# Kernel tuning notes

Hardware: AMD Instinct MI355X
Metric: run time of the kernel (lower is better)

## Reference

```python
import jax, jax.numpy as jnp
import numpy as np
from math import factorial, sqrt

# ---------------- irreps utilities ----------------
def parse(s):
    out = []
    for tok in s.split('+'):
        tok = tok.strip()
        mul, ir = (tok.split('x') if 'x' in tok else ('1', tok))
        out.append((int(mul), int(ir[:-1]), 1 if ir[-1] == 'e' else -1))
    return out

def irdim(ir):
    return sum(m * (2 * l + 1) for m, l, p in ir)

def slices(ir):
    s, o = [], 0
    for m, l, p in ir:
        s.append((o, m, l, p)); o += m * (2 * l + 1)
    return s

# ---------------- real Clebsch-Gordan coefficients ----------------
def _cgc(j1, m1, j2, m2, j3, m3):
    if m1 + m2 != m3:
        return 0.0
    f = factorial
    pre = sqrt((2 * j3 + 1) * f(j3 + j1 - j2) * f(j3 - j1 + j2) * f(j1 + j2 - j3) / f(j1 + j2 + j3 + 1))
    pre *= sqrt(f(j3 + m3) * f(j3 - m3) * f(j1 - m1) * f(j1 + m1) * f(j2 - m2) * f(j2 + m2))
    s = 0.0
    for k in range(max(0, j2 - j3 - m1, j1 - j3 + m2), min(j1 + j2 - j3, j1 - m1, j2 + m2) + 1):
        s += (-1) ** k / (f(k) * f(j1 + j2 - j3 - k) * f(j1 - m1 - k) * f(j2 + m2 - k) * f(j3 - j2 + m1 + k) * f(j3 - j1 - m2 + k))
    return pre * s

def _c2r(l):
    # complex -> real spherical-harmonic change of basis
    q = np.zeros((2 * l + 1, 2 * l + 1), dtype=complex); r2 = 1 / np.sqrt(2)
    q[l, l] = 1.0
    for mu in range(1, l + 1):
        q[mu + l, mu + l] = (-1) ** mu * r2; q[mu + l, -mu + l] = r2
        q[-mu + l, -mu + l] = 1j * r2;       q[-mu + l, mu + l] = -1j * (-1) ** mu * r2
    return q

_CGMEM = {}
def cg_real(l1, l2, l3):
    key = (l1, l2, l3)
    if key in _CGMEM:
        return _CGMEM[key]
    C = np.zeros((2 * l1 + 1, 2 * l2 + 1, 2 * l3 + 1))
    for m1 in range(-l1, l1 + 1):
        for m2 in range(-l2, l2 + 1):
            if abs(m1 + m2) <= l3:
                C[m1 + l1, m2 + l2, m1 + m2 + l3] = _cgc(l1, m1, l2, m2, l3, m1 + m2)
    T = np.einsum('am,bn,co,mno->abc', _c2r(l1), _c2r(l2), np.conj(_c2r(l3)), C)
    R = T.real if np.abs(T.real).sum() >= np.abs(T.imag).sum() else T.imag
    _CGMEM[key] = np.ascontiguousarray(R)
    return _CGMEM[key]

# ---------------- equivariant ops ----------------
def tp_paths(ir1, ir2, iro):
    P = []
    for (o1, m1, l1, p1) in slices(ir1):
        for (o2, m2, l2, p2) in slices(ir2):
            for (oo, mo, lo, po) in slices(iro):
                if po == p1 * p2 and abs(l1 - l2) <= lo <= l1 + l2:
                    P.append((o1, m1, l1, o2, m2, l2, oo, mo, lo))
    return P

def tp_numel(P):
    return sum(m1 * m2 * mo for (_, m1, _, _, m2, _, _, mo, _) in P)

def tp_apply(ir1, ir2, iro, x1, x2, w):
    # FullyConnectedTensorProduct with per-row (shared_weights=False) weights w:[E, numel]
    P = tp_paths(ir1, ir2, iro)
    out = jnp.zeros((x1.shape[0], irdim(iro)), x1.dtype)
    fan = {}
    for p in P:
        fan[p[6]] = fan.get(p[6], 0) + p[1] * p[4]
    off = 0
    for (o1, m1, l1, o2, m2, l2, oo, mo, lo) in P:
        cg = jnp.asarray(cg_real(l1, l2, lo), x1.dtype)
        a = x1[:, o1:o1 + m1 * (2 * l1 + 1)].reshape(-1, m1, 2 * l1 + 1)
        b = x2[:, o2:o2 + m2 * (2 * l2 + 1)].reshape(-1, m2, 2 * l2 + 1)
        ww = w[:, off:off + m1 * m2 * mo].reshape(-1, m1, m2, mo); off += m1 * m2 * mo
        r = jnp.einsum('eui,evj,euvw,ijk->ewk', a, b, ww, cg) / np.sqrt(fan[oo])
        out = out.at[:, oo:oo + mo * (2 * lo + 1)].add(r.reshape(-1, mo * (2 * lo + 1)))
    return out

def lin_pairs(iri, iro):
    return [(si, so) for si in slices(iri) for so in slices(iro) if si[2] == so[2] and si[3] == so[3]]

def lin_numel(iri, iro):
    return sum(si[1] * so[1] for si, so in lin_pairs(iri, iro))

def lin_apply(iri, iro, x, w):
    # o3.Linear: per-irrep channel mixing with fan-in normalization
    out = jnp.zeros((x.shape[0], irdim(iro)), x.dtype)
    pairs = lin_pairs(iri, iro)
    fan = {}
    for si, so in pairs:
        fan[so[0]] = fan.get(so[0], 0) + si[1]
    off = 0
    for (oi, mi, li, pi), (oo, mo, lo, po) in pairs:
        W = w[off:off + mi * mo].reshape(mi, mo); off += mi * mo
        xb = x[:, oi:oi + mi * (2 * li + 1)].reshape(-1, mi, 2 * li + 1)
        r = jnp.einsum('eui,uv->evi', xb, W) / np.sqrt(fan[oo])
        out = out.at[:, oo:oo + mo * (2 * lo + 1)].add(r.reshape(-1, mo * (2 * lo + 1)))
    return out

def act_apply(ir, acts, x):
    # tanh on scalar irreps only (flags in acts), identity elsewhere
    parts = []
    for (o, m, l, p), a in zip(slices(ir), acts):
        b = x[:, o:o + m * (2 * l + 1)]
        parts.append(jnp.tanh(b) if a else b)
    return jnp.concatenate(parts, axis=1)

def fc_apply(x, w, dims):
    # e3nn FullyConnectedNet: relu MLP with 1/sqrt(fan_in) weight normalization
    off, h = 0, x
    for i in range(len(dims) - 1):
        di, do = dims[i], dims[i + 1]
        W = w[off:off + di * do].reshape(di, do); off += di * do
        h = (h @ W) / np.sqrt(di)
        if i < len(dims) - 2:
            h = jax.nn.relu(h)
    return h

# ---------------- module irreps (from V_theta.__init__) ----------------
IRR_IN = parse('2x0e')
IRR_SH = parse('1x0e+1x1o+1x2e')
MID1 = parse('8x0e+8x1o+8x2e')
MID2 = parse('8x0e+8x0o+8x1e+8x1o+8x2e+8x2o')
IRR_HH = parse('4x0e+2x1o+2x1o+1x0e+1x1e+1x2e')
IRR_CC = parse('9x0e+6x1o+3x2e+6x1o+' + '1x0e+1x1e+1x2e+' * 4 + '1x1o+1x2o+1x3o+' * 2 + '3x2e+' + '1x1o+1x2o+1x3o+' * 2 + '1x0e+1x1e+1x2e+1x3e+1x4e')
IRR_CH = parse('6x0e+3x1o+4x1o+' + '1x0e+1x1e+1x2e+' * 2 + '2x2e+1x1o+1x2o+1x3o')
SCR = parse('32x0e+1x2e'); SCR2 = parse('1x0e+1x2e'); G1 = parse('32x0e'); G2 = parse('3x0e')
ACT2 = [1, 0, 0]; ACT3 = [1, 1, 0, 0, 0, 0]
P1 = tp_paths(IRR_IN, IRR_SH, MID1); P2 = tp_paths(MID1, IRR_SH, MID2); PB = tp_paths(MID2, MID2, MID2)
EMB_N = 16
FC1D = [1, EMB_N, EMB_N, EMB_N, tp_numel(P1)]
FC2D = [1, EMB_N, EMB_N, EMB_N, tp_numel(P2)]
FCBD = [1, EMB_N, EMB_N, EMB_N, tp_numel(PB)]

def fcsz(d):
    return sum(d[i] * d[i + 1] for i in range(len(d) - 1))

N_NODES, N_EDGES, N_BOND, SCALING = 10000, 100000, 1000, 0.2


def setup_inputs() -> dict:
    key = jax.random.key(0)
    ks = jax.random.split(key, 32)
    nrm = lambda i, shp: jax.random.normal(ks[i], shp, jnp.float32)
    return {
        'f_in': nrm(0, (N_NODES, 2)),
        'sh': nrm(1, (N_EDGES, 9)),
        'emb': jax.random.uniform(ks[2], (N_EDGES, 1), jnp.float32),
        'num_neighbors': jnp.full((1,), 10.0, jnp.float32),
        'w_lin1': nrm(3, (lin_numel(IRR_IN, IRR_IN),)),
        'w_lin2': nrm(4, (lin_numel(MID1, MID1),)),
        'w_lin3': nrm(5, (lin_numel(MID2, MID2),)),
        'w_linCC': nrm(6, (lin_numel(MID2, IRR_CC),)),
        'w_linHH': nrm(7, (lin_numel(MID2, IRR_HH),)),
        'w_linCH': nrm(8, (lin_numel(MID2, IRR_CH),)),
        'w_linC': nrm(9, (lin_numel(MID2, IRR_CC),)),
        'w_linH': nrm(10, (lin_numel(MID2, IRR_HH),)),
        'w_screen1': nrm(11, (lin_numel(MID2, SCR),)),
        'w_screen2': nrm(12, (lin_numel(SCR, SCR2),)),
        'w_gap1': nrm(13, (lin_numel(MID2, G1),)),
        'w_gap2': nrm(14, (lin_numel(G1, G2),)),
        'w_fc1': nrm(15, (fcsz(FC1D),)),
        'w_fc2': nrm(16, (fcsz(FC2D),)),
        'w_fcb': nrm(17, (fcsz(FCBD),)),
        'edge_src': jax.random.randint(ks[18], (N_EDGES,), 0, N_NODES),
        'edge_dst': jax.random.randint(ks[19], (N_EDGES,), 0, N_NODES),
        'HH_ind': jax.random.randint(ks[20], (N_BOND,), 0, N_EDGES),
        'CC_ind': jax.random.randint(ks[21], (N_BOND,), 0, N_EDGES),
        'CH_ind': jax.random.randint(ks[22], (N_BOND,), 0, N_EDGES),
        'num_nodes': N_NODES,
    }


def reference(f_in, sh, emb, num_neighbors, w_lin1, w_lin2, w_lin3, w_linCC, w_linHH, w_linCH, w_linC, w_linH, w_screen1, w_screen2, w_gap1, w_gap2, w_fc1, w_fc2, w_fcb, edge_src, edge_dst, HH_ind, CC_ind, CH_ind, num_nodes):
    inv = 1.0 / jnp.sqrt(num_neighbors)  # .div(num_neighbors**0.5)
    # layer 1: linear + tanh, gather -> TP with per-edge weights -> scatter-add
    x = jnp.tanh(lin_apply(IRR_IN, IRR_IN, f_in, w_lin1))
    ef = tp_apply(IRR_IN, IRR_SH, MID1, x[edge_src], sh, fc_apply(emb, w_fc1, FC1D))
    x = jax.ops.segment_sum(ef, edge_dst, num_segments=num_nodes) * inv
    x = act_apply(MID1, ACT2, lin_apply(MID1, MID1, x, w_lin2))
    # layer 2
    ef = tp_apply(MID1, IRR_SH, MID2, x[edge_src], sh, fc_apply(emb, w_fc2, FC2D))
    x = jax.ops.segment_sum(ef, edge_dst, num_segments=num_nodes) * inv
    x = act_apply(MID2, ACT3, lin_apply(MID2, MID2, x, w_lin3))
    # bond-level tensor products on edge subsets
    def bond(ind):
        return tp_apply(MID2, MID2, MID2, x[edge_src[ind]], x[edge_dst[ind]], fc_apply(emb[ind], w_fcb, FCBD))
    HHf, CCf, CHf = bond(HH_ind), bond(CC_ind), bond(CH_ind)
    eHH = lin_apply(MID2, IRR_HH, act_apply(MID2, ACT3, HHf), w_linHH)
    eCC = lin_apply(MID2, IRR_CC, act_apply(MID2, ACT3, CCf), w_linCC)
    eCH = lin_apply(MID2, IRR_CH, act_apply(MID2, ACT3, CHf), w_linCH)
    nC = lin_apply(MID2, IRR_CC, x, w_linC)
    nH = lin_apply(MID2, IRR_HH, x, w_linH)
    screen = lin_apply(SCR, SCR2, act_apply(SCR, [1, 0], lin_apply(MID2, SCR, x, w_screen1)), w_screen2)
    def gap(F):
        return lin_apply(G1, G2, jnp.tanh(lin_apply(MID2, G1, F, w_gap1)), w_gap2)
    s = SCALING
    # order: H, C, HH, CH, CC, screen, gap[CC], gap[HH], gap[CH]
    return (nH * s, nC * s, eHH * s, eCH * s, eCC * s, screen, gap(CCf), gap(HHf), gap(CHf))
```

## Files before the change

kernel.cpp:

```cpp
#include <hip/hip_runtime.h>
#include <hip/hip_bf16.h>

typedef __hip_bfloat16 bf16_t;

#define N_NODES 10000
#define N_EDGES 100000
#define N_BONDS 1000
#define RPW 4

__device__ __forceinline__ float bf2f(bf16_t v){ return __bfloat162float(v); }
__device__ __forceinline__ bf16_t f2bf(float v){ return __float2bfloat16(v); }
__device__ __forceinline__ int iabs(int x){ return x<0?-x:x; }

constexpr bool cg_nz(int l1,int l2,int l3,int i,int j,int k){
  int m1=i-l1, m2=j-l2, m3=k-l3;
  int neg=(m1<0)+(m2<0)+(m3<0);
  if (((neg ^ (l1+l2+l3)) & 1)!=0) return false;
  int a1=m1<0?-m1:m1, a2=m2<0?-m2:m2, a3=m3<0?-m3:m3;
  return (a3==a1+a2)||(a3==a1-a2)||(a3==a2-a1);
}

__device__ __forceinline__ void stout(void* out, size_t idx, float v, bool f32o){
  if (f32o) ((float*)out)[idx]=v;
  else      ((bf16_t*)out)[idx]=f2bf(v);
}

__global__ void detect_k(const unsigned short* nnb_raw, int* flag){
  *flag = (nnb_raw[0]==0x4120) ? 0 : 1;
}

struct CvtArgs {
  const void* src[19];
  float* dst[19];
  int n[19];
};

__global__ __launch_bounds__(256) void convert_k(CvtArgs a, const int* flag){
  bool f32 = (*flag)!=0;
  int tid = blockIdx.x*256+threadIdx.x;
  int nth = gridDim.x*256;
  for(int t=0;t<19;++t){
    int n=a.n[t];
    float* d=a.dst[t];
    if (f32){
      const float* s=(const float*)a.src[t];
      for(int i=tid;i<n;i+=nth) d[i]=s[i];
    } else {
      const bf16_t* s=(const bf16_t*)a.src[t];
      for(int i=tid;i<n;i+=nth) d[i]=bf2f(s[i]);
    }
  }
}

__global__ __launch_bounds__(256) void csr_count_k(const int* __restrict__ edst, int* __restrict__ cnt){
  int e=blockIdx.x*256+threadIdx.x; if(e>=N_EDGES) return;
  atomicAdd(&cnt[edst[e]],1);
}

__global__ __launch_bounds__(256) void csr_scan_k(const int* __restrict__ cnt,
    int* __restrict__ rowptr, int* __restrict__ pos){
  __shared__ int ssum[256];
  int t=threadIdx.x;
  int base=t*40;
  int s=0;
  for(int i=0;i<40;++i){ int idx=base+i; s += (idx<N_NODES)? cnt[idx]:0; }
  ssum[t]=s; __syncthreads();
  if(t==0){ int run=0; for(int i=0;i<256;++i){ int v=ssum[i]; ssum[i]=run; run+=v; } }
  __syncthreads();
  int run=ssum[t];
  for(int i=0;i<40;++i){
    int idx=base+i;
    if(idx<N_NODES){ rowptr[idx]=run; pos[idx]=run; run+=cnt[idx]; }
  }
  if(t==255) rowptr[N_NODES]=run;
}

__global__ __launch_bounds__(256) void csr_scatter_k(const int* __restrict__ edst,
    int* __restrict__ pos, int* __restrict__ sorted){
  int e=blockIdx.x*256+threadIdx.x; if(e>=N_EDGES) return;
  int p=atomicAdd(&pos[edst[e]],1);
  sorted[p]=e;
}

__device__ __forceinline__ double dfact(int n){
  const double F[11]={1.,1.,2.,6.,24.,120.,720.,5040.,40320.,362880.,3628800.};
  return F[n];
}

__device__ double cgc_d(int j1,int m1,int j2,int m2,int j3,int m3){
  if (m1+m2!=m3) return 0.0;
  double pre = sqrt((double)(2*j3+1)*dfact(j3+j1-j2)*dfact(j3-j1+j2)*dfact(j1+j2-j3)/dfact(j1+j2+j3+1));
  pre *= sqrt(dfact(j3+m3)*dfact(j3-m3)*dfact(j1-m1)*dfact(j1+m1)*dfact(j2-m2)*dfact(j2+m2));
  int k0 = max(0, max(j2-j3-m1, j1-j3+m2));
  int k1 = min(j1+j2-j3, min(j1-m1, j2+m2));
  double s=0.0;
  for(int k=k0;k<=k1;++k)
    s += ((k&1)?-1.0:1.0)/(dfact(k)*dfact(j1+j2-j3-k)*dfact(j1-m1-k)*dfact(j2+m2-k)*dfact(j3-j2+m1+k)*dfact(j3-j1-m2+k));
  return pre*s;
}

__device__ void c2r_d(int l,int a,int m,double&re,double&im){
  re=0.0; im=0.0;
  const double r2 = 0.7071067811865475244;
  int mu = a-l;
  if (mu==0){ if (m==l) re=1.0; return; }
  if (mu>0){
    if (m==l+mu) re = (mu&1)? -r2 : r2;
    else if (m==l-mu) re = r2;
  } else {
    int nu=-mu;
    if (m==l-nu) im = r2;
    else if (m==l+nu) im = (nu&1)? r2 : -r2;
  }
}

__global__ __launch_bounds__(128) void cg_init_k(float* cg){
  int b=blockIdx.x;
  int l1=b/9, l2=(b/3)%3, l3=b%3;
  if (l3 < iabs(l1-l2) || l3 > l1+l2) return;
  int n1=2*l1+1,n2=2*l2+1,n3=2*l3+1,n=n1*n2*n3;
  __shared__ double sRe[125], sIm[125];
  __shared__ int sPick;
  int t=threadIdx.x;
  if (t<n){
    int a=t/(n2*n3), bb=(t/n3)%n2, c=t%n3;
    double re=0.0, im=0.0;
    for(int m1=0;m1<n1;++m1){
      double q1r,q1i; c2r_d(l1,a,m1,q1r,q1i);
      if (q1r==0.0 && q1i==0.0) continue;
      for(int m2=0;m2<n2;++m2){
        double q2r,q2i; c2r_d(l2,bb,m2,q2r,q2i);
        if (q2r==0.0 && q2i==0.0) continue;
        int m3=(m1-l1)+(m2-l2)+l3;
        if (m3<0||m3>=n3) continue;
        double q3r,q3i; c2r_d(l3,c,m3,q3r,q3i); q3i=-q3i;
        double C = cgc_d(l1,m1-l1,l2,m2-l2,l3,m3-l3);
        if (C==0.0) continue;
        double ar = q1r*q2r - q1i*q2i;
        double ai = q1r*q2i + q1i*q2r;
        re += (ar*q3r - ai*q3i)*C;
        im += (ar*q3i + ai*q3r)*C;
      }
    }
    sRe[t]=re; sIm[t]=im;
  }
  __syncthreads();
  if (t==0){
    double s1=0.0,s2=0.0;
    for(int i=0;i<n;++i){ s1+=fabs(sRe[i]); s2+=fabs(sIm[i]); }
    sPick = (s1>=s2)?1:0;
  }
  __syncthreads();
  if (t<n) cg[b*125+t] = (float)(sPick? sRe[t] : sIm[t]);
}

__global__ __launch_bounds__(256) void nodeA_k(const float* __restrict__ fin,
                                               const float* __restrict__ w,
                                               float* __restrict__ x1){
  int n=blockIdx.x*256+threadIdx.x; if(n>=N_NODES) return;
  float f0=fin[2*n], f1=fin[2*n+1];
  const float r2=0.70710678f;
  x1[2*n]   = tanhf((f0*w[0]+f1*w[2])*r2);
  x1[2*n+1] = tanhf((f0*w[1]+f1*w[3])*r2);
}

__device__ __forceinline__ void mlp16(float e, const float* w, float* h){
  float a[16];
  #pragma unroll
  for(int j=0;j<16;++j) a[j]=fmaxf(e*w[j],0.f);
  float b[16];
  #pragma unroll
  for(int j=0;j<16;++j){
    float s=0.f;
    #pragma unroll
    for(int i=0;i<16;++i) s+=a[i]*w[16+i*16+j];
    b[j]=fmaxf(s*0.25f,0.f);
  }
  #pragma unroll
  for(int j=0;j<16;++j){
    float s=0.f;
    #pragma unroll
    for(int i=0;i<16;++i) s+=b[i]*w[272+i*16+j];
    h[j]=fmaxf(s*0.25f,0.f);
  }
}

__global__ __launch_bounds__(256) void hmlp_k(const float* __restrict__ emb,
    const float* __restrict__ wfc, float* __restrict__ H, int E){
  __shared__ float sw[528];
  for(int t=threadIdx.x;t<528;t+=256) sw[t]=wfc[t];
  __syncthreads();
  int e=blockIdx.x*256+threadIdx.x; if(e>=E) return;
  float h[16]; mlp16(emb[e], sw, h);
  float4* H4=(float4*)(H+(size_t)e*16);
  #pragma unroll
  for(int q=0;q<4;++q) H4[q]=make_float4(h[4*q],h[4*q+1],h[4*q+2],h[4*q+3]);
}

__global__ __launch_bounds__(256) void hb_k(const float* __restrict__ emb,
    const float* __restrict__ wfc, const int* __restrict__ i0,
    const int* __restrict__ i1, const int* __restrict__ i2,
    float* __restrict__ HB){
  __shared__ float sw[528];
  for(int t=threadIdx.x;t<528;t+=256) sw[t]=wfc[t];
  __syncthreads();
  int t=blockIdx.x*256+threadIdx.x; if(t>=3*N_BONDS) return;
  const int* ind = (t<N_BONDS)? i0 : (t<2*N_BONDS? i1 : i2);
  int ie = ind[t%N_BONDS];
  float h[16]; mlp16(emb[ie], sw, h);
  float4* H4=(float4*)(HB+(size_t)t*16);
  #pragma unroll
  for(int q=0;q<4;++q) H4[q]=make_float4(h[4*q],h[4*q+1],h[4*q+2],h[4*q+3]);
}

__global__ __launch_bounds__(256) void gemm16_k(const float* __restrict__ A,
    const float* __restrict__ B, float* __restrict__ C, int Eloc, int N,
    const int* __restrict__ idx){
  __shared__ float As[64][16];
  int tid=threadIdx.x;
  int et=blockIdx.x, ct=blockIdx.y;
  for(int t=tid;t<64*16;t+=256){
    int r=t/16, i=t%16;
    int e=et*64+r;
    int ea=(e<Eloc)? (idx? idx[e]:e) : -1;
    As[r][i]=(ea>=0)? A[(size_t)ea*16+i] : 0.f;
  }
  __syncthreads();
  int col=ct*64+(tid&63);
  int eq=tid>>6;
  bool colok = col<N;
  float Breg[16];
  #pragma unroll
  for(int i=0;i<16;++i) Breg[i]= colok? B[(size_t)i*N+col]*0.25f : 0.f;
  #pragma unroll 4
  for(int es=0;es<16;++es){
    int e=et*64+eq*16+es;
    if (e>=Eloc) break;
    float acc=0.f;
    #pragma unroll
    for(int i=0;i<16;++i) acc+=As[eq*16+es][i]*Breg[i];
    if (colok) C[(size_t)e*N+col]=acc;
  }
}

__global__ __launch_bounds__(256) void edge1b_k(const float* __restrict__ x1,
    const float* __restrict__ sh, const float* __restrict__ ww1,
    const int* __restrict__ esrc, const int* __restrict__ sorted,
    const int* __restrict__ rowptr, const float* __restrict__ nnb,
    float* __restrict__ xout){
  int tid=threadIdx.x;
  int n=blockIdx.x*32 + (tid>>3);
  int w8=tid&7;
  if (n>=N_NODES) return;
  float inv = rsqrtf(nnb[0]);
  const float c = 0.70710678f*inv;
  float acc[9];
  #pragma unroll
  for(int t=0;t<9;++t) acc[t]=0.f;
  int r0=rowptr[n], r1=rowptr[n+1];
  for(int r=r0;r<r1;++r){
    int e=sorted[r];
    int src=esrc[e];
    float a0=x1[2*src], a1=x1[2*src+1];
    const float* wr=ww1+(size_t)r*48;
    float w0=wr[w8],    w1=wr[8+w8];
    float w2=wr[16+w8], w3=wr[24+w8];
    float w4=wr[32+w8], w5=wr[40+w8];
    const float* b=sh+(size_t)e*9;
    float s0=w0*a0+w1*a1;
    acc[0]+=s0*b[0];
    float s1=w2*a0+w3*a1;
    #pragma unroll
    for(int j=0;j<3;++j) acc[1+j]+=s1*b[1+j];
    float s2=w4*a0+w5*a1;
    #pragma unroll
    for(int j=0;j<5;++j) acc[4+j]+=s2*b[4+j];
  }
  float* o=xout+(size_t)n*72;
  o[w8]=acc[0]*c;
  #pragma unroll
  for(int j=0;j<3;++j) o[8+w8*3+j]=acc[1+j]*c;
  #pragma unroll
  for(int j=0;j<5;++j) o[32+w8*5+j]=acc[4+j]*c;
}

__global__ __launch_bounds__(256) void lin2b_k(float* __restrict__ x, const float* __restrict__ w){
  __shared__ float sX[32*72];
  __shared__ float sW[192];
  int tid=threadIdx.x;
  int base=blockIdx.x*32;
  if (tid<192) sW[tid]=w[tid];
  for(int t=tid;t<32*72;t+=256){
    int n=base+t/72;
    sX[t] = (n<N_NODES)? x[(size_t)n*72 + t%72] : 0.f;
  }
  __syncthreads();
  int ns=tid>>3, v=tid&7;
  const float r8=0.35355339f;
  const float* X=sX+ns*72;
  float r[9];
  {
    float a=0.f;
    #pragma unroll
    for(int u=0;u<8;++u) a+=X[u]*sW[u*8+v];
    r[0]=tanhf(a*r8);
  }
  #pragma unroll
  for(int i=0;i<3;++i){
    float a=0.f;
    #pragma unroll
    for(int u=0;u<8;++u) a+=X[8+u*3+i]*sW[64+u*8+v];
    r[1+i]=a*r8;
  }
  #pragma unroll
  for(int i=0;i<5;++i){
    float a=0.f;
    #pragma unroll
    for(int u=0;u<8;++u) a+=X[32+u*5+i]*sW[128+u*8+v];
    r[4+i]=a*r8;
  }
  __syncthreads();
  float* Xw=sX+ns*72;
  Xw[v]=r[0];
  #pragma unroll
  for(int i=0;i<3;++i) Xw[8+v*3+i]=r[1+i];
  #pragma unroll
  for(int i=0;i<5;++i) Xw[32+v*5+i]=r[4+i];
  __syncthreads();
  for(int t=tid;t<32*72;t+=256){
    int n=base+t/72;
    if (n<N_NODES) x[(size_t)n*72 + t%72]=sX[t];
  }
}

__global__ __launch_bounds__(256) void lin3b_k(float* __restrict__ x, const float* __restrict__ w){
  __shared__ float sX[32*144];
  __shared__ float sW[384];
  int tid=threadIdx.x;
  int base=blockIdx.x*32;
  for(int t=tid;t<384;t+=256) sW[t]=w[t];
  for(int t=tid;t<32*144;t+=256){
    int n=base+t/144;
    sX[t] = (n<N_NODES)? x[(size_t)n*144 + t%144] : 0.f;
  }
  __syncthreads();
  int ns=tid>>3, v=tid&7;
  const float r8=0.35355339f;
  const float* X=sX+ns*144;
  float r[18];
  {
    float a=0.f;
    #pragma unroll
    for(int u=0;u<8;++u) a+=X[u]*sW[u*8+v];
    r[0]=tanhf(a*r8);
  }
  {
    float a=0.f;
    #pragma unroll
    for(int u=0;u<8;++u) a+=X[8+u]*sW[64+u*8+v];
    r[1]=tanhf(a*r8);
  }
  #pragma unroll
  for(int i=0;i<3;++i){
    float a=0.f;
    #pragma unroll
    for(int u=0;u<8;++u) a+=X[16+u*3+i]*sW[128+u*8+v];
    r[2+i]=a*r8;
  }
  #pragma unroll
  for(int i=0;i<3;++i){
    float a=0.f;
    #pragma unroll
    for(int u=0;u<8;++u) a+=X[40+u*3+i]*sW[192+u*8+v];
    r[5+i]=a*r8;
  }
  #pragma unroll
  for(int i=0;i<5;++i){
    float a=0.f;
    #pragma unroll
    for(int u=0;u<8;++u) a+=X[64+u*5+i]*sW[256+u*8+v];
    r[8+i]=a*r8;
  }
  #pragma unroll
  for(int i=0;i<5;++i){
    float a=0.f;
    #pragma unroll
    for(int u=0;u<8;++u) a+=X[104+u*5+i]*sW[320+u*8+v];
    r[13+i]=a*r8;
  }
  __syncthreads();
  float* Xw=sX+ns*144;
  Xw[v]=r[0];
  Xw[8+v]=r[1];
  #pragma unroll
  for(int i=0;i<3;++i) Xw[16+v*3+i]=r[2+i];
  #pragma unroll
  for(int i=0;i<3;++i) Xw[40+v*3+i]=r[5+i];
  #pragma unroll
  for(int i=0;i<5;++i) Xw[64+v*5+i]=r[8+i];
  #pragma unroll
  for(int i=0;i<5;++i) Xw[104+v*5+i]=r[13+i];
  __syncthreads();
  for(int t=tid;t<32*144;t+=256){
    int n=base+t/144;
    if (n<N_NODES) x[(size_t)n*144 + t%144]=sX[t];
  }
}

template<int L1,int L2,int LO,int BO,int SLOT>
__device__ __forceinline__ void tp_acc(const float* Au, const float* b,
    const float* __restrict__ cg, float wv, float* acc){
  constexpr int D1=2*L1+1, D2=2*L2+1, DN=2*LO+1;
  const float* C = cg + ((L1*3+L2)*3+LO)*125;
  float P[DN];
  #pragma unroll
  for(int k=0;k<DN;++k) P[k]=0.f;
  #pragma unroll
  for(int i=0;i<D1;++i){
    float av=Au[i];
    #pragma unroll
    for(int j=0;j<D2;++j){
      #pragma unroll
      for(int k=0;k<DN;++k){
        if (cg_nz(L1,L2,LO,i,j,k)){
          float cv=C[(i*D2+j)*DN+k];
          P[k]+=av*(cv*b[BO+j]);
        }
      }
    }
  }
  #pragma unroll
  for(int k=0;k<DN;++k) acc[SLOT+k]+=wv*P[k];
}

__device__ __forceinline__ void e2_finish2(float* acc, float inv, float* __restrict__ o, bool first){
  int lane=threadIdx.x&63;
  int w=lane&7;
  #pragma unroll
  for(int t=0;t<18;++t){
    acc[t]+=__shfl_xor(acc[t],8,64);
    acc[t]+=__shfl_xor(acc[t],16,64);
    acc[t]+=__shfl_xor(acc[t],32,64);
  }
  if (lane<8){
    float f0 =rsqrtf(24.f)*inv;
    float f1e=rsqrtf(16.f)*inv;
    float f1o=rsqrtf(32.f)*inv;
    float f2e=rsqrtf(32.f)*inv;
    float f2o=rsqrtf(16.f)*inv;
    if (first){
      o[0+w]=acc[0]*f0;
      o[8+w]=0.f;
      #pragma unroll
      for(int k=0;k<3;++k) o[16+w*3+k]=acc[2+k]*f1e;
      #pragma unroll
      for(int k=0;k<3;++k) o[40+w*3+k]=acc[5+k]*f1o;
      #pragma unroll
      for(int k=0;k<5;++k) o[64+w*5+k]=acc[8+k]*f2e;
      #pragma unroll
      for(int k=0;k<5;++k) o[104+w*5+k]=acc[13+k]*f2o;
    } else {
      o[0+w]+=acc[0]*f0;
      #pragma unroll
      for(int k=0;k<3;++k) o[16+w*3+k]+=acc[2+k]*f1e;
      #pragma unroll
      for(int k=0;k<3;++k) o[40+w*3+k]+=acc[5+k]*f1o;
      #pragma unroll
      for(int k=0;k<5;++k) o[64+w*5+k]+=acc[8+k]*f2e;
      #pragma unroll
      for(int k=0;k<5;++k) o[104+w*5+k]+=acc[13+k]*f2o;
    }
  }
}

__device__ __forceinline__ void e2_flush(float* acc, float inv, float* __restrict__ o){
  int lane=threadIdx.x&63;
  int w=lane&7;
  #pragma unroll
  for(int t=0;t<18;++t){
    acc[t]+=__shfl_xor(acc[t],8,64);
    acc[t]+=__shfl_xor(acc[t],16,64);
    acc[t]+=__shfl_xor(acc[t],32,64);
  }
  if (lane<8){
    float f0 =rsqrtf(24.f)*inv;
    float f1e=rsqrtf(16.f)*inv;
    float f1o=rsqrtf(32.f)*inv;
    float f2e=rsqrtf(32.f)*inv;
    float f2o=rsqrtf(16.f)*inv;
    atomicAdd(&o[0+w], acc[0]*f0);
    #pragma unroll
    for(int k=0;k<3;++k) atomicAdd(&o[16+w*3+k], acc[2+k]*f1e);
    #pragma unroll
    for(int k=0;k<3;++k) atomicAdd(&o[40+w*3+k], acc[5+k]*f1o);
    #pragma unroll
    for(int k=0;k<5;++k) atomicAdd(&o[64+w*5+k], acc[8+k]*f2e);
    #pragma unroll
    for(int k=0;k<5;++k) atomicAdd(&o[104+w*5+k], acc[13+k]*f2o);
  }
}

__device__ __forceinline__ void e2c_consume(const float* __restrict__ xn,
    const float* __restrict__ sh, const float* __restrict__ cg,
    const float* wwp, int e, int src, int u, int lane, float* acc){
  float sv[15];
  sv[ 0]=wwp[  0+lane]; sv[ 1]=wwp[256+lane]; sv[ 2]=wwp[768+lane];
  sv[ 3]=wwp[320+lane]; sv[ 4]=wwp[832+lane];
  sv[ 5]=wwp[ 64+lane]; sv[ 6]=wwp[192+lane]; sv[ 7]=wwp[448+lane]; sv[ 8]=wwp[640+lane];
  sv[ 9]=wwp[128+lane]; sv[10]=wwp[384+lane]; sv[11]=wwp[576+lane]; sv[12]=wwp[896+lane];
  sv[13]=wwp[512+lane]; sv[14]=wwp[704+lane];
  const float* A = xn + (size_t)src*72;
  float b[9];
  #pragma unroll
  for(int j=0;j<9;++j) b[j]=sh[(size_t)e*9+j];
  float a0[1]; a0[0]=A[u];
  float a1[3];
  #pragma unroll
  for(int i=0;i<3;++i) a1[i]=A[8+u*3+i];
  float a2[5];
  #pragma unroll
  for(int i=0;i<5;++i) a2[i]=A[32+u*5+i];
  tp_acc<0,0,0,0, 0>(a0,b,cg,sv[ 0],acc);
  tp_acc<1,1,0,1, 0>(a1,b,cg,sv[ 1],acc);
  tp_acc<2,2,0,4, 0>(a2,b,cg,sv[ 2],acc);
  tp_acc<1,1,1,1, 2>(a1,b,cg,sv[ 3],acc);
  tp_acc<2,2,1,4, 2>(a2,b,cg,sv[ 4],acc);
  tp_acc<0,1,1,1, 5>(a0,b,cg,sv[ 5],acc);
  tp_acc<1,0,1,0, 5>(a1,b,cg,sv[ 6],acc);
  tp_acc<1,2,1,4, 5>(a1,b,cg,sv[ 7],acc);
  tp_acc<2,1,1,1, 5>(a2,b,cg,sv[ 8],acc);
  tp_acc<0,2,2,4, 8>(a0,b,cg,sv[ 9],acc);
  tp_acc<1,1,2,1, 8>(a1,b,cg,sv[10],acc);
  tp_acc<2,0,2,0, 8>(a2,b,cg,sv[11],acc);
  tp_acc<2,2,2,4, 8>(a2,b,cg,sv[12],acc);
  tp_acc<1,2,2,4,13>(a1,b,cg,sv[13],acc);
  tp_acc<2,1,2,1,13>(a2,b,cg,sv[14],acc);
}

__global__ __launch_bounds__(256) void edge2r_k(const float* __restrict__ xn,
    const float* __restrict__ sh, const float* __restrict__ ww2,
    const int* __restrict__ esrc, const int* __restrict__ sorted,
    const int* __restrict__ rowptr, const float* __restrict__ nnb,
    const float* __restrict__ cg, float* __restrict__ xout,
    int rb, int re){
  int gw=blockIdx.x*4+(threadIdx.x>>6);
  int lane=threadIdx.x&63;
  int u=lane>>3;
  int rs=rb+gw*RPW;
  if (rs>=re) return;
  int rend=min(rs+RPW, re);
  float inv=rsqrtf(nnb[0]);
  int lo=0, hi=N_NODES-1;
  while(lo<hi){ int mid=(lo+hi+1)>>1; if(rowptr[mid]<=rs) lo=mid; else hi=mid-1; }
  int n=lo;
  int nend=rowptr[n+1];
  float acc[18];
  #pragma unroll
  for(int t=0;t<18;++t) acc[t]=0.f;
  bool dirty=false;
  for(int r=rs;r<rend;++r){
    while(r>=nend){
      if (dirty){
        e2_flush(acc, inv, xout+(size_t)n*144);
        #pragma unroll
        for(int t=0;t<18;++t) acc[t]=0.f;
        dirty=false;
      }
      n++; nend=rowptr[n+1];
    }
    int e=__builtin_amdgcn_readfirstlane(sorted[r]);
    int src=__builtin_amdgcn_readfirstlane(esrc[e]);
    e2c_consume(xn,sh,cg, ww2+(size_t)(r-rb)*960, e,src,u,lane,acc);
    dirty=true;
  }
  if (dirty) e2_flush(acc, inv, xout+(size_t)n*144);
}

__global__ __launch_bounds__(256) void edge2c_k(const float* __restrict__ xn,
    const float* __restrict__ sh, const float* __restrict__ h2,
    const float* __restrict__ Wg, const int* __restrict__ esrc,
    const int* __restrict__ sorted, const int* __restrict__ rowptr,
    const float* __restrict__ nnb, const float* __restrict__ cg,
    float* __restrict__ xout){
  __shared__ float ww[2][4][960];
  __shared__ int sE[4];
  __shared__ int sCnt[4];
  int tid=threadIdx.x, wid=tid>>6, lane=tid&63;
  int n=blockIdx.x*4+wid;
  int u=lane>>3;
  float inv=rsqrtf(nnb[0]);
  int r0=rowptr[n], r1=rowptr[n+1];
  if (lane==0) sCnt[wid]=r1-r0;
  __syncthreads();
  int mx = max(max(sCnt[0],sCnt[1]),max(sCnt[2],sCnt[3]));
  float acc[18];
  #pragma unroll
  for(int t=0;t<18;++t) acc[t]=0.f;
  int pe=0, psrc=0; bool pact=false;
  for(int t=0;t<mx;++t){
    int r=r0+t;
    bool act=(r<r1);
    int e=0, src=0;
    if (act){
      e=__builtin_amdgcn_readfirstlane(sorted[r]);
      src=__builtin_amdgcn_readfirstlane(esrc[e]);
    }
    if (lane==0) sE[wid]= act? e : -1;
    __syncthreads();
    if (tid<240){
      int e0=max(sE[0],0), e1=max(sE[1],0), e2i=max(sE[2],0), e3=max(sE[3],0);
      const float* h0=h2+(size_t)e0*16;
      const float* h1=h2+(size_t)e1*16;
      const float* hq=h2+(size_t)e2i*16;
      const float* h3=h2+(size_t)e3*16;
      float4 av[4];
      #pragma unroll
      for(int k=0;k<4;++k) av[k]=make_float4(0.f,0.f,0.f,0.f);
      #pragma unroll
      for(int i=0;i<16;++i){
        float hx=h0[i], hy=h1[i], hz=hq[i], hw=h3[i];
        const float* Wr=Wg+i*960;
        #pragma unroll
        for(int k=0;k<4;++k){
          float w=Wr[tid+240*k];
          av[k].x+=hx*w; av[k].y+=hy*w; av[k].z+=hz*w; av[k].w+=hw*w;
        }
      }
      float* wb=&ww[t&1][0][0];
      #pragma unroll
      for(int k=0;k<4;++k){
        int c=tid+240*k;
        wb[c]=av[k].x*0.25f; wb[960+c]=av[k].y*0.25f;
        wb[1920+c]=av[k].z*0.25f; wb[2880+c]=av[k].w*0.25f;
      }
    }
    if (pact){
      const float* wwp=&ww[(t&1)^1][wid][0];
      e2c_consume(xn,sh,cg,wwp,pe,psrc,u,lane,acc);
    }
    pe=e; psrc=src; pact=act;
    __syncthreads();
  }
  if (pact){
    const float* wwp=&ww[(mx-1)&1][wid][0];
    e2c_consume(xn,sh,cg,wwp,pe,psrc,u,lane,acc);
  }
  e2_finish2(acc, inv, xout+(size_t)n*144, true);
}

struct IrS{ short off,m,l,p; };
__device__ const IrS SL_MID2[6]={{0,8,0,1},{8,8,0,-1},{16,8,1,1},{40,8,1,-1},{64,8,2,1},{104,8,2,-1}};
__device__ const IrS SL_HH[6]={{0,4,0,1},{4,2,1,-1},{10,2,1,-1},{16,1,0,1},{17,1,1,1},{20,1,2,1}};
__device__ const IrS SL_CC[34]={{0,9,0,1},{9,6,1,-1},{27,3,2,1},{42,6,1,-1},
 {60,1,0,1},{61,1,1,1},{64,1,2,1},{69,1,0,1},{70,1,1,1},{73,1,2,1},
 {78,1,0,1},{79,1,1,1},{82,1,2,1},{87,1,0,1},{88,1,1,1},{91,1,2,1},
 {96,1,1,-1},{99,1,2,-1},{104,1,3,-1},{111,1,1,-1},{114,1,2,-1},{119,1,3,-1},
 {126,3,2,1},{141,1,1,-1},{144,1,2,-1},{149,1,3,-1},{156,1,1,-1},{159,1,2,-1},{164,1,3,-1},
 {171,1,0,1},{172,1,1,1},{175,1,2,1},{180,1,3,1},{187,1,4,1}};
__device__ const IrS SL_CH[13]={{0,6,0,1},{6,3,1,-1},{15,4,1,-1},{27,1,0,1},{28,1,1,1},{31,1,2,1},
 {36,1,0,1},{37,1,1,1},{40,1,2,1},{45,2,2,1},{55,1,1,-1},{58,1,2,-1},{63,1,3,-1}};

__device__ void lin_out_r(const float* __restrict__ x, bool act16, const float* __restrict__ w,
                          const IrS* so, int no, void* out, size_t base, bool f32o,
                          float scale, int aBeg, int aEnd, bool zf){
  float tx[16];
  bool need_tx = act16 && (aBeg<2);
  if (need_tx){
    #pragma unroll
    for(int i=0;i<16;++i) tx[i]=tanhf(x[i]);
  }
  if (zf){
    for(int bI=0;bI<no;++bI){
      if (so[bI].l>=3){
        int cnt=so[bI].m*(2*so[bI].l+1);
        for(int t=0;t<cnt;++t) stout(out, base+so[bI].off+t, 0.f, f32o);
      }
    }
  }
  int woff=0;
  float f = 0.35355339f*scale;
  for(int a=0;a<6;++a){
    int la=SL_MID2[a].l, pa=SL_MID2[a].p, oa=SL_MID2[a].off;
    int d=2*la+1;
    bool doit = (a>=aBeg && a<aEnd);
    for(int bI=0;bI<no;++bI){
      if (so[bI].l!=la || so[bI].p!=pa) continue;
      int mo=so[bI].m;
      if (doit){
        for(int v=0;v<mo;++v){
          for(int i=0;i<d;++i){
            float acc=0.f;
            for(int u=0;u<8;++u){
              int idx=oa+u*d+i;
              float xv=(act16 && idx<16)? tx[idx] : x[idx];
              acc+=xv*w[woff+u*mo+v];
            }
            stout(out, base+so[bI].off+v*d+i, acc*f, f32o);
          }
        }
      }
      woff+=8*mo;
    }
  }
}

__global__ __launch_bounds__(256) void node_out_k(const float* __restrict__ x,
    const float* __restrict__ wC, const float* __restrict__ wH,
    const float* __restrict__ ws1, const float* __restrict__ ws2,
    void* out, const int* __restrict__ flag){
  int tid=threadIdx.x;
  int gw=blockIdx.x*4+(tid>>6);
  int lane=tid&63;
  int job=gw&7;
  int n=(gw>>3)*64+lane;
  if (n>=N_NODES) return;
  bool f32o = (*flag)!=0;
  const float* X = x + (size_t)n*144;
  if (job==0){
    lin_out_r(X,false,wH,SL_HH,6, out, (size_t)n*25, f32o, 0.2f, 0,6, true);
  } else if (job==1){
    const float r8=0.35355339f, r32=0.17677670f;
    float t0[32];
    for(int v=0;v<32;++v){
      float acc=0.f;
      #pragma unroll
      for(int u=0;u<8;++u) acc+=X[u]*ws1[u*32+v];
      t0[v]=tanhf(acc*r8);
    }
    float t2[5];
    #pragma unroll
    for(int i=0;i<5;++i){
      float acc=0.f;
      #pragma unroll
      for(int u=0;u<8;++u) acc+=X[64+u*5+i]*ws1[256+u];
      t2[i]=acc*r8;
    }
    size_t sb = 2501000 + (size_t)n*6;
    float acc=0.f;
    for(int v=0;v<32;++v) acc+=t0[v]*ws2[v];
    stout(out, sb, acc*r32, f32o);
    float w2e=ws2[32];
    #pragma unroll
    for(int i=0;i<5;++i) stout(out, sb+1+i, t2[i]*w2e, f32o);
  } else {
    int a=job-2;
    lin_out_r(X,false,wC,SL_CC,34, out, 250000 + (size_t)n*196, f32o, 0.2f,
              a, a+1, a==0);
  }
}

template<int L1,int L2,int LO>
__device__ __forceinline__ void bond_path2(const float* sa,int ao,const float* sb,int bo,
    const float* __restrict__ cg, const float* __restrict__ wwp,
    float invfan, float* sF, int oo, int lane){
  constexpr int D1=2*L1+1, D2=2*L2+1, DN=2*LO+1;
  const float* C = cg + ((L1*3+L2)*3+LO)*125;
  int u=lane>>3, v=lane&7;
  float P[DN];
  #pragma unroll
  for(int k=0;k<DN;++k) P[k]=0.f;
  #pragma unroll
  for(int i=0;i<D1;++i){
    float avv=sa[ao+u*D1+i];
    #pragma unroll
    for(int j=0;j<D2;++j){
      #pragma unroll
      for(int k=0;k<DN;++k){
        if (cg_nz(L1,L2,LO,i,j,k)){
          float cv=C[(i*D2+j)*DN+k];
          P[k]+=(avv*sb[bo+v*D2+j])*cv;
        }
      }
    }
  }
  int v2=u;
  float acc[DN];
  #pragma unroll
  for(int k=0;k<DN;++k) acc[k]=0.f;
  #pragma unroll
  for(int u2=0;u2<8;++u2){
    float ww=wwp[u2*64 + lane];
    int srcl=u2*8+v2;
    #pragma unroll
    for(int k=0;k<DN;++k) acc[k]+=ww*__shfl(P[k],srcl,64);
  }
  #pragma unroll
  for(int k=0;k<DN;++k){
    acc[k]+=__shfl_xor(acc[k],8,64);
    acc[k]+=__shfl_xor(acc[k],16,64);
    acc[k]+=__shfl_xor(acc[k],32,64);
  }
  int w=lane&7;
  if (v2==0){
    #pragma unroll
    for(int k=0;k<DN;++k) sF[oo+w*DN+k]+=acc[k]*invfan;
  }
}

__device__ __forceinline__ void bond_disp(int code, const float* a,int ao,const float* bb,int bo,
    const float* __restrict__ cg, const float* __restrict__ wwp,
    float fv, float* Ff, int oo, int lane){
  switch(code){
    case 0:  bond_path2<0,0,0>(a,ao,bb,bo,cg,wwp,fv,Ff,oo,lane); break;
    case 4:  bond_path2<0,1,1>(a,ao,bb,bo,cg,wwp,fv,Ff,oo,lane); break;
    case 8:  bond_path2<0,2,2>(a,ao,bb,bo,cg,wwp,fv,Ff,oo,lane); break;
    case 10: bond_path2<1,0,1>(a,ao,bb,bo,cg,wwp,fv,Ff,oo,lane); break;
    case 12: bond_path2<1,1,0>(a,ao,bb,bo,cg,wwp,fv,Ff,oo,lane); break;
    case 13: bond_path2<1,1,1>(a,ao,bb,bo,cg,wwp,fv,Ff,oo,lane); break;
    case 14: bond_path2<1,1,2>(a,ao,bb,bo,cg,wwp,fv,Ff,oo,lane); break;
    case 16: bond_path2<1,2,1>(a,ao,bb,bo,cg,wwp,fv,Ff,oo,lane); break;
    case 17: bond_path2<1,2,2>(a,ao,bb,bo,cg,wwp,fv,Ff,oo,lane); break;
    case 20: bond_path2<2,0,2>(a,ao,bb,bo,cg,wwp,fv,Ff,oo,lane); break;
    case 22: bond_path2<2,1,1>(a,ao,bb,bo,cg,wwp,fv,Ff,oo,lane); break;
    case 23: bond_path2<2,1,2>(a,ao,bb,bo,cg,wwp,fv,Ff,oo,lane); break;
    case 24: bond_path2<2,2,0>(a,ao,bb,bo,cg,wwp,fv,Ff,oo,lane); break;
    case 25: bond_path2<2,2,1>(a,ao,bb,bo,cg,wwp,fv,Ff,oo,lane); break;
    case 26: bond_path2<2,2,2>(a,ao,bb,bo,cg,wwp,fv,Ff,oo,lane); break;
  }
}

__global__ __launch_bounds__(256) void bond_tpl_k(const float* __restrict__ xn,
    const float* __restrict__ hb, const float* __restrict__ Wg,
    const int* __restrict__ esrc, const int* __restrict__ edst,
    const int* __restrict__ i0, const int* __restrict__ i1,
    const int* __restrict__ i2, const float* __restrict__ cg,
    float* __restrict__ F0, float* __restrict__ F1, float* __restrict__ F2){
  __shared__ float sA[4][144], sB[4][144], sF[4][144];
  __shared__ float ww[2][2048];
  int tid=threadIdx.x;
  int wid=tid>>6, lane=tid&63;
  int gb=blockIdx.x*4+wid;
  int s=gb/N_BONDS, bi=gb-s*N_BONDS;
  const int* ind=(s==0)?i0:(s==1)?i1:i2;
  float* F=(s==0)?F0:(s==1)?F1:F2;
  int ie=ind[bi];
  int src=esrc[ie], dst=edst[ie];
  for(int t=lane;t<144;t+=64){
    sA[wid][t]=xn[(size_t)src*144+t];
    sB[wid][t]=xn[(size_t)dst*144+t];
    sF[wid][t]=0.f;
  }
  float4 hreg[16];
  {
    size_t hbase=(size_t)blockIdx.x*64;
    #pragma unroll
    for(int i=0;i<16;++i)
      hreg[i]=make_float4(hb[hbase+i],hb[hbase+16+i],hb[hbase+32+i],hb[hbase+48+i]);
  }
  const int SL_L[6]={0,0,1,1,2,2};
  const int SL_P[6]={1,-1,1,-1,1,-1};
  const int SL_O[6]={0,8,16,40,64,104};
  const float fi0=rsqrtf(384.f), fi1=rsqrtf(768.f);
  int pidx=0;
  int pcode=0, pao=0, pbo=0, poo=0; float pfv=0.f;
  for(int s1=0;s1<6;++s1){
    for(int s2=0;s2<6;++s2){
      for(int so=0;so<6;++so){
        int l1=SL_L[s1], l2=SL_L[s2], lo=SL_L[so];
        if (SL_P[so]!=SL_P[s1]*SL_P[s2]) continue;
        if (lo<iabs(l1-l2) || lo>l1+l2) continue;
        {
          const float* Wp = Wg + (size_t)pidx*512 + 2*tid;
          float4 a0=make_float4(0.f,0.f,0.f,0.f);
          float4 a1=make_float4(0.f,0.f,0.f,0.f);
          #pragma unroll
          for(int i=0;i<16;++i){
            float2 wv = *(const float2*)(Wp + (size_t)i*30720);
            float4 h=hreg[i];
            a0.x+=h.x*wv.x; a0.y+=h.y*wv.x; a0.z+=h.z*wv.x; a0.w+=h.w*wv.x;
            a1.x+=h.x*wv.y; a1.y+=h.y*wv.y; a1.z+=h.z*wv.y; a1.w+=h.w*wv.y;
          }
          float* wb=ww[pidx&1];
          int c=2*tid;
          *(float2*)(wb+0*512+c)=make_float2(a0.x*0.25f, a1.x*0.25f);
          *(float2*)(wb+1*512+c)=make_float2(a0.y*0.25f, a1.y*0.25f);
          *(float2*)(wb+2*512+c)=make_float2(a0.z*0.25f, a1.z*0.25f);
          *(float2*)(wb+3*512+c)=make_float2(a0.w*0.25f, a1.w*0.25f);
        }
        if (pidx>0){
          const float* wwp = ww[(pidx-1)&1] + wid*512;
          bond_disp(pcode, sA[wid], pao, sB[wid], pbo, cg, wwp, pfv, sF[wid], poo, lane);
        }
        pcode=l1*9+l2*3+lo; pao=SL_O[s1]; pbo=SL_O[s2]; poo=SL_O[so];
        pfv=(lo==0)? fi0 : fi1;
        pidx++;
        __syncthreads();
      }
    }
  }
  {
    const float* wwp = ww[(pidx-1)&1] + wid*512;
    bond_disp(pcode, sA[wid], pao, sB[wid], pbo, cg, wwp, pfv, sF[wid], poo, lane);
  }
  __syncthreads();
  for(int t=lane;t<144;t+=64) F[(size_t)bi*144+t]=sF[wid][t];
}

__global__ __launch_bounds__(256) void bond_out3_k(
    const float* __restrict__ F0, const float* __restrict__ F1,
    const float* __restrict__ F2,
    const float* __restrict__ wHH, const float* __restrict__ wCC,
    const float* __restrict__ wCH,
    const float* __restrict__ wg1, const float* __restrict__ wg2,
    void* out, const int* __restrict__ flag){
  int tbl=blockIdx.x>>5;
  int blk=blockIdx.x&31;
  int tid=threadIdx.x;
  int gw=blk*4+(tid>>6);
  int lane=tid&63;
  int job=gw&7;
  int n=(gw>>3)*64+lane;
  if (n>=N_BONDS) return;
  bool f32o = (*flag)!=0;
  const float* F = (tbl==0)?F0:(tbl==1)?F1:F2;
  const float* wlin = (tbl==0)?wHH:(tbl==1)?wCC:wCH;
  size_t baseE = (tbl==0)?2210000u:(tbl==1)?2305000u:2235000u;
  size_t baseG = (tbl==0)?2564000u:(tbl==1)?2561000u:2567000u;
  const float* X=F+(size_t)n*144;
  if (job==0){
    const float r8=0.35355339f, r32=0.17677670f;
    float g[32];
    for(int v=0;v<32;++v){
      float acc=0.f;
      #pragma unroll
      for(int u=0;u<8;++u) acc+=X[u]*wg1[u*32+v];
      g[v]=tanhf(acc*r8);
    }
    #pragma unroll
    for(int c=0;c<3;++c){
      float acc=0.f;
      for(int v=0;v<32;++v) acc+=g[v]*wg2[v*3+c];
      stout(out, baseG+(size_t)n*3+c, acc*r32, f32o);
    }
  } else if (job>=2){
    const IrS* so; int no; int dim;
    if(tbl==0){so=SL_HH;no=6;dim=25;}
    else if(tbl==1){so=SL_CC;no=34;dim=196;}
    else {so=SL_CH;no=13;dim=70;}
    int a=job-2;
    lin_out_r(X,true,wlin,so,no,out,baseE+(size_t)n*dim,f32o,0.2f,
              a, a+1, a==0);
  }
}

extern "C" void kernel_launch(void* const* d_in, const int* in_sizes, int n_in,
                              void* d_out, int out_size, void* d_ws, size_t ws_size,
                              hipStream_t stream){
  const int* esrc=(const int*)d_in[19];
  const int* edst=(const int*)d_in[20];
  const int* iHH =(const int*)d_in[21];
  const int* iCC =(const int*)d_in[22];
  const int* iCH =(const int*)d_in[23];
  float* ws=(float*)d_ws;
  int* flag=(int*)d_ws;

  size_t off=16;
  auto alloc=[&](size_t n){ size_t o=off; off+=(n+15)&~(size_t)15; return o; };
  size_t o_cg = alloc(27*125);
  size_t o_st[19];
  for(int i=0;i<19;++i) o_st[i]=alloc((size_t)in_sizes[i]);
  size_t o_xM1 = alloc(720000);
  size_t o_xM2 = alloc(1440000);
  size_t o_h2  = alloc((size_t)N_EDGES*16);
  size_t o_hb  = alloc((size_t)3*N_BONDS*16);
  size_t o_cnt = alloc(10016);
  size_t o_rp  = alloc(10016);
  size_t o_pos = alloc(10016);
  size_t o_srt = alloc(N_EDGES);
  size_t o_x1  = alloc(20000);
  size_t o_F0  = alloc(144000);
  size_t o_F1  = alloc(144000);
  size_t o_F2  = alloc(144000);
  size_t o_h1  = alloc((size_t)N_EDGES*16);
  size_t o_ww1 = alloc((size_t)N_EDGES*48);
  (void)o_ww1;

  float* cg  = ws+o_cg;
  float* x1  = ws+o_x1;
  float* xM1 = ws+o_xM1;
  float* xM2 = ws+o_xM2;
  float* F0  = ws+o_F0;
  float* F1  = ws+o_F1;
  float* F2  = ws+o_F2;
  float* h1  = ws+o_h1;
  float* h2  = ws+o_h2;
  float* hb  = ws+o_hb;
  float* ww1 = ws+o_ww1;
  int* cnt   = (int*)(ws+o_cnt);
  int* rowptr= (int*)(ws+o_rp);
  int* pos   = (int*)(ws+o_pos);
  int* sorted= (int*)(ws+o_srt);

  size_t totf = ws_size/sizeof(float);
  size_t availf = (totf>o_x1)? totf-o_x1 : 0;
  int CHUNK = (int)((availf/960 < (size_t)N_EDGES)? availf/960 : (size_t)N_EDGES);
  bool use_chunk = (CHUNK >= 2000);
  float* ww2 = ws + o_x1;

  CvtArgs ca;
  for(int i=0;i<19;++i){ ca.src[i]=d_in[i]; ca.dst[i]=ws+o_st[i]; ca.n[i]=in_sizes[i]; }
  const float* f_in   = ws+o_st[0];
  const float* sh     = ws+o_st[1];
  const float* emb    = ws+o_st[2];
  const float* nnb    = ws+o_st[3];
  const float* w_lin1 = ws+o_st[4];
  const float* w_lin2 = ws+o_st[5];
  const float* w_lin3 = ws+o_st[6];
  const float* w_linCC= ws+o_st[7];
  const float* w_linHH= ws+o_st[8];
  const float* w_linCH= ws+o_st[9];
  const float* w_linC = ws+o_st[10];
  const float* w_linH = ws+o_st[11];
  const float* w_s1   = ws+o_st[12];
  const float* w_s2   = ws+o_st[13];
  const float* w_g1   = ws+o_st[14];
  const float* w_g2   = ws+o_st[15];
  const float* w_fc1  = ws+o_st[16];
  const float* w_fc2  = ws+o_st[17];
  const float* w_fcb  = ws+o_st[18];

  detect_k<<<1,1,0,stream>>>((const unsigned short*)d_in[3], flag);
  convert_k<<<512,256,0,stream>>>(ca, flag);
  cg_init_k<<<27,128,0,stream>>>(cg);
  hipMemsetAsync(cnt, 0, 10000*sizeof(int), stream);
  csr_count_k<<<391,256,0,stream>>>(edst, cnt);
  csr_scan_k<<<1,256,0,stream>>>(cnt, rowptr, pos);
  csr_scatter_k<<<391,256,0,stream>>>(edst, pos, sorted);

  nodeA_k<<<40,256,0,stream>>>(f_in,w_lin1,x1);
  hmlp_k<<<391,256,0,stream>>>(emb, w_fc1, h1, N_EDGES);
  hmlp_k<<<391,256,0,stream>>>(emb, w_fc2, h2, N_EDGES);
  hb_k<<<12,256,0,stream>>>(emb, w_fcb, iHH, iCC, iCH, hb);

  gemm16_k<<<dim3(1563,1),256,0,stream>>>(h1, w_fc1+528, ww1, N_EDGES, 48, sorted);
  edge1b_k<<<313,256,0,stream>>>(x1,sh,ww1,esrc,sorted,rowptr,nnb,xM1);
  lin2b_k<<<313,256,0,stream>>>(xM1,w_lin2);

  if (use_chunk){
    hipMemsetAsync(xM2, 0, 1440000*sizeof(float), stream);
    int nch = (N_EDGES + CHUNK - 1)/CHUNK;
    for (int ci=0; ci<nch; ++ci){
      int rb = ci*CHUNK;
      int re = rb+CHUNK; if (re>N_EDGES) re=N_EDGES;
      int Cc = re-rb;
      gemm16_k<<<dim3((Cc+63)/64,15),256,0,stream>>>(h2, w_fc2+528, ww2, Cc, 960, sorted+rb);
      int waves=(Cc+RPW-1)/RPW;
      int blocks=(waves+3)/4;
      edge2r_k<<<blocks,256,0,stream>>>(xM1, sh, ww2, esrc, sorted, rowptr,
          nnb, cg, xM2, rb, re);
    }
  } else {
    edge2c_k<<<2500,256,0,stream>>>(xM1, sh, h2, w_fc2+528,
        esrc, sorted, rowptr, nnb, cg, xM2);
  }
  lin3b_k<<<313,256,0,stream>>>(xM2,w_lin3);
  node_out_k<<<314,256,0,stream>>>(xM2,w_linC,w_linH,w_s1,w_s2,d_out,flag);

  bond_tpl_k<<<750,256,0,stream>>>(xM2, hb, w_fcb+528,
      esrc, edst, iHH, iCC, iCH, cg, F0, F1, F2);

  bond_out3_k<<<96,256,0,stream>>>(F0,F1,F2,w_linHH,w_linCC,w_linCH,
      w_g1,w_g2,d_out,flag);
}
```

Before: 875.4 us.

## Fuse dtype detection and MLP kernels, halve rows per wave, coalesce bond weight loads

Folds the one-thread dtype detection kernel into the conversion kernel and merges three small MLP launches into one combined grid, cutting launch overhead. Changes RPW from 4 to 2, giving edge2r more waves with fewer rows each. Bond weight-generation loads and stores switch from strided float2 accesses to contiguous scalar accesses at tid and tid+256 for better coalescing and fewer LDS bank conflicts. The RPW change shifts the balance between parallelism and per-wave reuse in the hot edge kernel.

```diff
diff --git a/kernel.cpp b/kernel.cpp
--- a/kernel.cpp
+++ b/kernel.cpp
@@ -6,7 +6,7 @@
 #define N_NODES 10000
 #define N_EDGES 100000
 #define N_BONDS 1000
-#define RPW 4
+#define RPW 2
 
 __device__ __forceinline__ float bf2f(bf16_t v){ return __bfloat162float(v); }
 __device__ __forceinline__ bf16_t f2bf(float v){ return __float2bfloat16(v); }
@@ -25,18 +25,16 @@
   else      ((bf16_t*)out)[idx]=f2bf(v);
 }
 
-__global__ void detect_k(const unsigned short* nnb_raw, int* flag){
-  *flag = (nnb_raw[0]==0x4120) ? 0 : 1;
-}
-
 struct CvtArgs {
   const void* src[19];
   float* dst[19];
   int n[19];
 };
 
-__global__ __launch_bounds__(256) void convert_k(CvtArgs a, const int* flag){
-  bool f32 = (*flag)!=0;
+__global__ __launch_bounds__(256) void convert_k(CvtArgs a,
+    const unsigned short* __restrict__ nnb_raw, int* flag){
+  bool f32 = (nnb_raw[0]!=0x4120);
+  if (blockIdx.x==0 && threadIdx.x==0) *flag = f32?1:0;
   int tid = blockIdx.x*256+threadIdx.x;
   int nth = gridDim.x*256;
   for(int t=0;t<19;++t){
@@ -185,30 +183,36 @@
   }
 }
 
-__global__ __launch_bounds__(256) void hmlp_k(const float* __restrict__ emb,
-    const float* __restrict__ wfc, float* __restrict__ H, int E){
+__global__ __launch_bounds__(256) void mlps_k(const float* __restrict__ emb,
+    const float* __restrict__ wfc1, const float* __restrict__ wfc2,
+    const float* __restrict__ wfcb,
+    const int* __restrict__ i0, const int* __restrict__ i1,
+    const int* __restrict__ i2,
+    float* __restrict__ H1, float* __restrict__ H2, float* __restrict__ HB){
   __shared__ float sw[528];
+  int b=blockIdx.x;
+  const float* wfc; float* H; int eidx; bool ok;
+  if (b<391){
+    wfc=wfc1; H=H1;
+    int e=b*256+threadIdx.x; ok=(e<N_EDGES); eidx= ok? e:0;
+  } else if (b<782){
+    wfc=wfc2; H=H2;
+    int e=(b-391)*256+threadIdx.x; ok=(e<N_EDGES); eidx= ok? e:0;
+  } else {
+    wfc=wfcb; H=HB;
+    int t=(b-782)*256+threadIdx.x; ok=(t<3*N_BONDS);
+    eidx=0;
+    if (ok){
+      const int* ind = (t<N_BONDS)? i0 : (t<2*N_BONDS? i1 : i2);
+      eidx = ind[t%N_BONDS];
+    }
+  }
   for(int t=threadIdx.x;t<528;t+=256) sw[t]=wfc[t];
   __syncthreads();
-  int e=blockIdx.x*256+threadIdx.x; if(e>=E) return;
-  float h[16]; mlp16(emb[e], sw, h);
-  float4* H4=(float4*)(H+(size_t)e*16);
-  #pragma unroll
-  for(int q=0;q<4;++q) H4[q]=make_float4(h[4*q],h[4*q+1],h[4*q+2],h[4*q+3]);
-}
-
-__global__ __launch_bounds__(256) void hb_k(const float* __restrict__ emb,
-    const float* __restrict__ wfc, const int* __restrict__ i0,
-    const int* __restrict__ i1, const int* __restrict__ i2,
-    float* __restrict__ HB){
-  __shared__ float sw[528];
-  for(int t=threadIdx.x;t<528;t+=256) sw[t]=wfc[t];
-  __syncthreads();
-  int t=blockIdx.x*256+threadIdx.x; if(t>=3*N_BONDS) return;
-  const int* ind = (t<N_BONDS)? i0 : (t<2*N_BONDS? i1 : i2);
-  int ie = ind[t%N_BONDS];
-  float h[16]; mlp16(emb[ie], sw, h);
-  float4* H4=(float4*)(HB+(size_t)t*16);
+  if (!ok) return;
+  int orow = (b<782)? eidx : ((b-782)*256+threadIdx.x);
+  float h[16]; mlp16(emb[eidx], sw, h);
+  float4* H4=(float4*)(H+(size_t)orow*16);
   #pragma unroll
   for(int q=0;q<4;++q) H4[q]=make_float4(h[4*q],h[4*q+1],h[4*q+2],h[4*q+3]);
 }
@@ -860,22 +864,26 @@
         if (SL_P[so]!=SL_P[s1]*SL_P[s2]) continue;
         if (lo<iabs(l1-l2) || lo>l1+l2) continue;
         {
-          const float* Wp = Wg + (size_t)pidx*512 + 2*tid;
+          const float* Wp = Wg + (size_t)pidx*512;
           float4 a0=make_float4(0.f,0.f,0.f,0.f);
           float4 a1=make_float4(0.f,0.f,0.f,0.f);
           #pragma unroll
           for(int i=0;i<16;++i){
-            float2 wv = *(const float2*)(Wp + (size_t)i*30720);
+            float w0=Wp[(size_t)i*30720 + tid];
+            float w1=Wp[(size_t)i*30720 + tid + 256];
             float4 h=hreg[i];
-            a0.x+=h.x*wv.x; a0.y+=h.y*wv.x; a0.z+=h.z*wv.x; a0.w+=h.w*wv.x;
-            a1.x+=h.x*wv.y; a1.y+=h.y*wv.y; a1.z+=h.z*wv.y; a1.w+=h.w*wv.y;
+            a0.x+=h.x*w0; a0.y+=h.y*w0; a0.z+=h.z*w0; a0.w+=h.w*w0;
+            a1.x+=h.x*w1; a1.y+=h.y*w1; a1.z+=h.z*w1; a1.w+=h.w*w1;
           }
           float* wb=ww[pidx&1];
-          int c=2*tid;
-          *(float2*)(wb+0*512+c)=make_float2(a0.x*0.25f, a1.x*0.25f);
-          *(float2*)(wb+1*512+c)=make_float2(a0.y*0.25f, a1.y*0.25f);
-          *(float2*)(wb+2*512+c)=make_float2(a0.z*0.25f, a1.z*0.25f);
-          *(float2*)(wb+3*512+c)=make_float2(a0.w*0.25f, a1.w*0.25f);
+          wb[0*512+tid]    =a0.x*0.25f;
+          wb[1*512+tid]    =a0.y*0.25f;
+          wb[2*512+tid]    =a0.z*0.25f;
+          wb[3*512+tid]    =a0.w*0.25f;
+          wb[0*512+tid+256]=a1.x*0.25f;
+          wb[1*512+tid+256]=a1.y*0.25f;
+          wb[2*512+tid+256]=a1.z*0.25f;
+          wb[3*512+tid+256]=a1.w*0.25f;
         }
         if (pidx>0){
           const float* wwp = ww[(pidx-1)&1] + wid*512;
@@ -1019,8 +1027,7 @@
   const float* w_fc2  = ws+o_st[17];
   const float* w_fcb  = ws+o_st[18];
 
-  detect_k<<<1,1,0,stream>>>((const unsigned short*)d_in[3], flag);
-  convert_k<<<512,256,0,stream>>>(ca, flag);
+  convert_k<<<512,256,0,stream>>>(ca, (const unsigned short*)d_in[3], flag);
   cg_init_k<<<27,128,0,stream>>>(cg);
   hipMemsetAsync(cnt, 0, 10000*sizeof(int), stream);
   csr_count_k<<<391,256,0,stream>>>(edst, cnt);
@@ -1028,9 +1035,7 @@
   csr_scatter_k<<<391,256,0,stream>>>(edst, pos, sorted);
 
   nodeA_k<<<40,256,0,stream>>>(f_in,w_lin1,x1);
-  hmlp_k<<<391,256,0,stream>>>(emb, w_fc1, h1, N_EDGES);
-  hmlp_k<<<391,256,0,stream>>>(emb, w_fc2, h2, N_EDGES);
-  hb_k<<<12,256,0,stream>>>(emb, w_fcb, iHH, iCC, iCH, hb);
+  mlps_k<<<794,256,0,stream>>>(emb, w_fc1, w_fc2, w_fcb, iHH, iCC, iCH, h1, h2, hb);
 
   gemm16_k<<<dim3(1563,1),256,0,stream>>>(h1, w_fc1+528, ww1, N_EDGES, 48, sorted);
   edge1b_k<<<313,256,0,stream>>>(x1,sh,ww1,esrc,sorted,rowptr,nnb,xM1);
```

After: 934.2 us. 1.07x slower.
